# Kernel tuning notes

Measured on AMD Instinct MI355X. Metric: run time of the kernel, lower is better.

## Reference

```python
import jax, jax.numpy as jnp
import numpy as np

B = 1024        # sessions
N = 32          # nodes per session
S = 50          # steps per session
H = 256         # hidden_size
V = 50000       # vocab size of embedding_table
GROUP = 3       # items pooled per step (reshape(-1, 3, H) in source)
SAN_BLOCKS = 3


def setup_inputs() -> dict:
    key = jax.random.key(0)
    ks = jax.random.split(key, 16)
    node_embedding = jax.random.normal(ks[0], (B * N, H), jnp.float32)
    emb_weight = jax.random.normal(ks[1], (V, H), jnp.float32) * 0.02
    batch = jnp.repeat(jnp.arange(B, dtype=jnp.int32), N)           # session id per node
    sequence = jax.random.randint(ks[2], (B * S, GROUP), 0, N + 1)  # local idx; ==N -> zero pad row
    itemset_len = jax.random.randint(ks[3], (B * S,), 1, GROUP + 1).astype(jnp.float32)
    sequence_len = jnp.full((B,), S, dtype=jnp.int32)               # steps per session
    cue = jax.random.randint(ks[4], (B,), 0, V)
    sc = 1.0 / np.sqrt(H)
    in_proj_w = jax.random.normal(ks[5], (3 * H, H), jnp.float32) * sc
    in_proj_b = jnp.zeros((3 * H,), jnp.float32)
    out_proj_w = jax.random.normal(ks[6], (H, H), jnp.float32) * sc
    out_proj_b = jnp.zeros((H,), jnp.float32)
    d1_w = jax.random.normal(ks[7], (H, H), jnp.float32) * sc
    d1_b = jnp.zeros((H,), jnp.float32)
    d2_w = jax.random.normal(ks[8], (H, H), jnp.float32) * sc
    d2_b = jnp.zeros((H,), jnp.float32)
    W3_w = jax.random.normal(ks[9], (H, 2 * H), jnp.float32) * (1.0 / np.sqrt(2 * H))
    W3_b = jnp.zeros((H,), jnp.float32)
    return {
        "node_embedding": node_embedding, "emb_weight": emb_weight,
        "itemset_len": itemset_len, "in_proj_w": in_proj_w, "in_proj_b": in_proj_b,
        "out_proj_w": out_proj_w, "out_proj_b": out_proj_b,
        "d1_w": d1_w, "d1_b": d1_b, "d2_w": d2_w, "d2_b": d2_b,
        "W3_w": W3_w, "W3_b": W3_b,
        "batch": batch, "sequence": sequence, "sequence_len": sequence_len, "cue": cue,
    }


def reference(node_embedding, emb_weight, itemset_len, in_proj_w, in_proj_b,
              out_proj_w, out_proj_b, d1_w, d1_b, d2_w, d2_b, W3_w, W3_b,
              batch, sequence, sequence_len, cue):
    # Eval mode: dropout disabled.
    total_nodes, h = node_embedding.shape
    nsess = sequence_len.shape[0]
    total_steps = sequence.shape[0]

    # Per-session node counts and exclusive offsets (replaces torch.split on ragged batch).
    sections = jnp.bincount(batch, length=nsess)
    offsets = jnp.cumsum(sections) - sections

    # Append one global zero row; local index == sections[sess] maps to it
    # (matches the per-session zero row in v_i_zeros).
    nodes_pad = jnp.concatenate([node_embedding, jnp.zeros((1, h), node_embedding.dtype)], axis=0)
    step_sess = jnp.repeat(jnp.arange(nsess), sequence_len, total_repeat_length=total_steps)
    sec_s = sections[step_sess][:, None]
    off_s = offsets[step_sess][:, None]
    gidx = jnp.where(sequence == sec_s, total_nodes, off_s + sequence)  # [T, 3] global indices

    # session_i: 3-way sum of gathered node embeddings / itemset_len  -> [T, H]
    step_emb = nodes_pad[gidx].sum(axis=1) / itemset_len[:, None]

    # Last step of each session (both v_n and the position s_g is read from).
    last_idx = jnp.cumsum(sequence_len) - 1
    v_n = step_emb[last_idx]  # [B, H]

    # nn.MultiheadAttention receives (L=1, N=steps, E=H): softmax over a single key
    # is identically 1, so MHA == out_proj(v_proj(x)) applied per step independently.
    # Hence the SAN chain on the last step equals the chain applied to v_n alone.
    Wv = in_proj_w[2 * h:]
    bv = in_proj_b[2 * h:]
    x = v_n
    for _ in range(SAN_BLOCKS):
        attn = (x @ Wv.T + bv) @ out_proj_w.T + out_proj_b
        # Residual FFN (dropout off in eval): x + d2(relu(d1(x)))
        x = attn + (jax.nn.relu(attn @ d1_w.T + d1_b) @ d2_w.T + d2_b)
    s_g = x  # [B, H]

    s_h = jnp.concatenate([v_n, s_g], axis=1) @ W3_w.T + W3_b  # [B, H]
    y_hat = jnp.sum(s_h * emb_weight[cue], axis=1)             # [B]
    all_scores = s_h @ emb_weight.T                            # [B, V]
    return y_hat, all_scores
```

## Files before the change

kernel.cpp:

```cpp
#include <hip/hip_runtime.h>
#include <hip/hip_bf16.h>
#include <stdint.h>

typedef __attribute__((ext_vector_type(8))) short short8;
typedef __attribute__((ext_vector_type(4))) short short4v;
typedef __attribute__((ext_vector_type(4))) float f32x4;

#define HD 256

__device__ __forceinline__ ushort f2bf(float f) {
  union { float f; uint32_t u; } x; x.f = f;
  uint32_t r = (x.u + 0x7fffu + ((x.u >> 16) & 1u)) >> 16;
  return (ushort)r;
}

__device__ __forceinline__ int swz(int row, int col) {
  int chunk = (col >> 3) ^ (row & 7);
  return row * 256 + chunk * 8 + (col & 7);
}

__global__ void prep1_kernel(const int* __restrict__ batch, int total_nodes,
                             int* __restrict__ sections,
                             const float* __restrict__ in_proj_w,
                             const float* __restrict__ out_proj_w,
                             const float* __restrict__ d1_w,
                             const float* __restrict__ d2_w,
                             const float* __restrict__ W3_w,
                             ushort* __restrict__ Wv_bf, ushort* __restrict__ Po_bf,
                             ushort* __restrict__ d1_bf, ushort* __restrict__ d2_bf,
                             ushort* __restrict__ W3_bf) {
  int stride = gridDim.x * blockDim.x;
  int t0 = blockIdx.x * blockDim.x + threadIdx.x;
  for (int i = t0; i < total_nodes; i += stride)
    atomicAdd(&sections[batch[i]], 1);
  for (int i = t0; i < HD * HD; i += stride) {
    Wv_bf[i] = f2bf(in_proj_w[2 * HD * HD + i]);
    Po_bf[i] = f2bf(out_proj_w[i]);
    d1_bf[i] = f2bf(d1_w[i]);
    d2_bf[i] = f2bf(d2_w[i]);
  }
  for (int i = t0; i < HD * 2 * HD; i += stride)
    W3_bf[i] = f2bf(W3_w[i]);
}

__global__ void scan_kernel(const int* __restrict__ seq_len, int* __restrict__ sections,
                            int* __restrict__ offsets, int* __restrict__ last_idx,
                            int nsess) {
  __shared__ int s1[1024];
  __shared__ int s2[1024];
  int t = threadIdx.x;
  int v1 = (t < nsess) ? sections[t] : 0;
  int v2 = (t < nsess) ? seq_len[t] : 0;
  s1[t] = v1; s2[t] = v2;
  for (int d = 1; d < 1024; d <<= 1) {
    __syncthreads();
    int a1 = (t >= d) ? s1[t - d] : 0;
    int a2 = (t >= d) ? s2[t - d] : 0;
    __syncthreads();
    s1[t] += a1; s2[t] += a2;
  }
  __syncthreads();
  if (t < nsess) {
    offsets[t] = s1[t] - v1;
    last_idx[t] = s2[t] - 1;
  }
}

template<bool RELU, bool RESID, bool WACC>
__device__ __forceinline__ void gemm_stage16(const ushort* inA, const ushort* __restrict__ Wbf,
                                             const float* __restrict__ bias,
                                             float* accf, ushort* outB) {
  int t = threadIdx.x;
  int lane = t & 63, wid = t >> 6;
  int la = lane & 15, g = lane >> 4;
  int col = wid * 16 + la;
  f32x4 acc = {0.f, 0.f, 0.f, 0.f};
#pragma unroll
  for (int kk = 0; kk < 8; ++kk) {
    short8 a = *(const short8*)&inA[swz(la, kk * 32 + g * 8)];
    short8 b = *(const short8*)&Wbf[col * HD + kk * 32 + g * 8];
    acc = __builtin_amdgcn_mfma_f32_16x16x32_bf16(a, b, acc, 0, 0, 0);
  }
  float bia = bias[col];
#pragma unroll
  for (int r = 0; r < 4; ++r) {
    int ro = g * 4 + r;
    float v = acc[r] + bia;
    if (RELU) v = fmaxf(v, 0.f);
    if (RESID) v += accf[ro * HD + col];
    if (WACC) accf[ro * HD + col] = v;
    outB[swz(ro, col)] = f2bf(v);
  }
}

__device__ __forceinline__ void stage_fence() {
  __syncthreads();
  __builtin_amdgcn_sched_barrier(0);
}

__global__ __launch_bounds__(1024, 1) void sh_kernel(
    const float* __restrict__ node_emb, const float* __restrict__ emb_w,
    const float* __restrict__ itemset_len, const float* __restrict__ in_proj_b,
    const float* __restrict__ out_proj_b, const float* __restrict__ d1_b,
    const float* __restrict__ d2_b, const float* __restrict__ W3_b,
    const int* __restrict__ sequence, const int* __restrict__ cue,
    const int* __restrict__ sections, const int* __restrict__ offsets,
    const int* __restrict__ last_idx,
    const ushort* __restrict__ Wv_bf, const ushort* __restrict__ Po_bf,
    const ushort* __restrict__ d1_bf, const ushort* __restrict__ d2_bf,
    const ushort* __restrict__ W3_bf,
    ushort* __restrict__ sh_bf, float* __restrict__ y_hat, int group) {
  __shared__ float accf[16 * HD];
  __shared__ ushort vn_bf[16 * HD];
  __shared__ ushort bufA[16 * HD];
  __shared__ ushort bufB[16 * HD];
  int t = threadIdx.x;
  int b0 = blockIdx.x * 16;

  {
    int r = t >> 6, cg = t & 63;
    int sess = b0 + r;
    int li = last_idx[sess];
    float inv = 1.0f / itemset_len[li];
    int sec = sections[sess], off = offsets[sess];
    float4 s = {0.f, 0.f, 0.f, 0.f};
    for (int gi = 0; gi < group; ++gi) {
      int sq = sequence[li * group + gi];
      if (sq == sec) continue;
      float4 v = *(const float4*)(node_emb + (size_t)(off + sq) * HD + cg * 4);
      s.x += v.x; s.y += v.y; s.z += v.z; s.w += v.w;
    }
    short4v u;
    u[0] = (short)f2bf(s.x * inv); u[1] = (short)f2bf(s.y * inv);
    u[2] = (short)f2bf(s.z * inv); u[3] = (short)f2bf(s.w * inv);
    *(short4v*)&vn_bf[swz(r, cg * 4)] = u;
  }
  stage_fence();

  const ushort* cur = vn_bf;
#pragma unroll 1
  for (int sb = 0; sb < 3; ++sb) {
    gemm_stage16<false, false, false>(cur, Wv_bf, in_proj_b + 2 * HD, nullptr, bufA);
    stage_fence();
    gemm_stage16<false, false, true>(bufA, Po_bf, out_proj_b, accf, bufB);
    stage_fence();
    gemm_stage16<true, false, false>(bufB, d1_bf, d1_b, nullptr, bufA);
    stage_fence();
    gemm_stage16<false, true, false>(bufA, d2_bf, d2_b, accf, bufB);
    stage_fence();
    cur = bufB;
  }

  {
    int lane = t & 63, wid = t >> 6;
    int la = lane & 15, g = lane >> 4;
    int col = wid * 16 + la;
    f32x4 acc = {0.f, 0.f, 0.f, 0.f};
#pragma unroll
    for (int kk = 0; kk < 16; ++kk) {
      const ushort* src = (kk < 8) ? vn_bf : cur;
      short8 a = *(const short8*)&src[swz(la, (kk & 7) * 32 + g * 8)];
      short8 b = *(const short8*)&W3_bf[col * 2 * HD + kk * 32 + g * 8];
      acc = __builtin_amdgcn_mfma_f32_16x16x32_bf16(a, b, acc, 0, 0, 0);
    }
    float bia = W3_b[col];
#pragma unroll
    for (int r = 0; r < 4; ++r) {
      int ro = g * 4 + r;
      float v = acc[r] + bia;
      accf[ro * HD + col] = v;
      sh_bf[(size_t)(b0 + ro) * HD + col] = f2bf(v);
    }
  }
  stage_fence();

  {
    int r = t >> 6, lane = t & 63;
    const float4 er = *(const float4*)(emb_w + (size_t)cue[b0 + r] * HD + lane * 4);
    const float* ar = &accf[r * HD + lane * 4];
    float p = ar[0] * er.x + ar[1] * er.y + ar[2] * er.z + ar[3] * er.w;
#pragma unroll
    for (int off = 32; off >= 1; off >>= 1) p += __shfl_down(p, off, 64);
    if (lane == 0) y_hat[b0 + r] = p;
  }
}

__global__ __launch_bounds__(256) void score_kernel(
    const ushort* __restrict__ sh_bf, const float* __restrict__ emb_w,
    float* __restrict__ scores, int nrows, int V) {
  __shared__ ushort ebuf[64 * HD];
  int t = threadIdx.x;
  int c0 = blockIdx.x * 64;
#pragma unroll
  for (int i = 0; i < 8; ++i) {
    int c = t + i * 256;
    int row = c >> 5, q = c & 31;
    if (c0 + row < V) {
      const float4* src = (const float4*)(emb_w + (size_t)(c0 + row) * HD + q * 8);
      float4 v0 = src[0], v1 = src[1];
      short8 u;
      u[0] = (short)f2bf(v0.x); u[1] = (short)f2bf(v0.y);
      u[2] = (short)f2bf(v0.z); u[3] = (short)f2bf(v0.w);
      u[4] = (short)f2bf(v1.x); u[5] = (short)f2bf(v1.y);
      u[6] = (short)f2bf(v1.z); u[7] = (short)f2bf(v1.w);
      *(short8*)&ebuf[row * 256 + ((q ^ (row & 7)) * 8)] = u;
    }
  }
  __syncthreads();

  int lane = t & 63, wid = t >> 6;
  int la = lane & 15, g = lane >> 4;
  int nrb = nrows >> 6;
  for (int rb = 0; rb < nrb; ++rb) {
    int r0 = rb * 64 + wid * 16;
    const ushort* arow = sh_bf + (size_t)(r0 + la) * HD;
    short8 a[8];
#pragma unroll
    for (int kk = 0; kk < 8; ++kk) a[kk] = *(const short8*)&arow[kk * 32 + g * 8];
    f32x4 acc[4] = {{0.f,0.f,0.f,0.f},{0.f,0.f,0.f,0.f},{0.f,0.f,0.f,0.f},{0.f,0.f,0.f,0.f}};
#pragma unroll
    for (int kk = 0; kk < 8; ++kk) {
#pragma unroll
      for (int ct = 0; ct < 4; ++ct) {
        int brow = ct * 16 + la;
        short8 b = *(const short8*)&ebuf[brow * 256 + (((kk * 4 + g) ^ (brow & 7)) * 8)];
        acc[ct] = __builtin_amdgcn_mfma_f32_16x16x32_bf16(a[kk], b, acc[ct], 0, 0, 0);
      }
    }
#pragma unroll
    for (int ct = 0; ct < 4; ++ct) {
      int col = c0 + ct * 16 + la;
      if (col < V) {
#pragma unroll
        for (int r = 0; r < 4; ++r) {
          int m = r0 + g * 4 + r;
          scores[(size_t)m * V + col] = acc[ct][r];
        }
      }
    }
  }
}

extern "C" void kernel_launch(void* const* d_in, const int* in_sizes, int n_in,
                              void* d_out, int out_size, void* d_ws, size_t ws_size,
                              hipStream_t stream) {
  const float* node_emb   = (const float*)d_in[0];
  const float* emb_w      = (const float*)d_in[1];
  const float* itemset_len= (const float*)d_in[2];
  const float* in_proj_w  = (const float*)d_in[3];
  const float* in_proj_b  = (const float*)d_in[4];
  const float* out_proj_w = (const float*)d_in[5];
  const float* out_proj_b = (const float*)d_in[6];
  const float* d1_w       = (const float*)d_in[7];
  const float* d1_b       = (const float*)d_in[8];
  const float* d2_w       = (const float*)d_in[9];
  const float* d2_b       = (const float*)d_in[10];
  const float* W3_w       = (const float*)d_in[11];
  const float* W3_b       = (const float*)d_in[12];
  const int*   batch      = (const int*)d_in[13];
  const int*   sequence   = (const int*)d_in[14];
  const int*   seq_len    = (const int*)d_in[15];
  const int*   cue        = (const int*)d_in[16];

  int total_nodes = in_sizes[0] / HD;
  int V           = in_sizes[1] / HD;
  int nsess       = in_sizes[15];
  int total_steps = in_sizes[2];
  int group       = in_sizes[14] / total_steps;

  char* ws = (char*)d_ws;
  int* sections   = (int*)(ws);
  int* offsets    = (int*)(ws + 4096);
  int* last_idx   = (int*)(ws + 8192);
  ushort* sh_bf   = (ushort*)(ws + 16384);
  ushort* Wv_bf   = (ushort*)(ws + 16384 + 524288);
  ushort* Po_bf   = Wv_bf + HD * HD;
  ushort* d1_bf   = Po_bf + HD * HD;
  ushort* d2_bf   = d1_bf + HD * HD;
  ushort* W3_bf   = d2_bf + HD * HD;

  float* y_hat  = (float*)d_out;
  float* scores = (float*)d_out + nsess;

  hipMemsetAsync(sections, 0, (size_t)nsess * sizeof(int), stream);
  prep1_kernel<<<512, 256, 0, stream>>>(batch, total_nodes, sections,
                                        in_proj_w, out_proj_w, d1_w, d2_w, W3_w,
                                        Wv_bf, Po_bf, d1_bf, d2_bf, W3_bf);
  scan_kernel<<<1, 1024, 0, stream>>>(seq_len, sections, offsets, last_idx, nsess);
  sh_kernel<<<nsess / 16, 1024, 0, stream>>>(node_emb, emb_w, itemset_len, in_proj_b,
                                             out_proj_b, d1_b, d2_b, W3_b,
                                             sequence, cue, sections, offsets, last_idx,
                                             Wv_bf, Po_bf, d1_bf, d2_bf, W3_bf,
                                             sh_bf, y_hat, group);
  score_kernel<<<(V + 63) / 64, 256, 0, stream>>>(sh_bf, emb_w, scores, nsess, V);
}
```

Before: 162.8 us.

## Fold V/out projections into one matrix, binary-search sections, vectorize score stores

Precomputes Wc = out_proj·Wv and a combined bias on device, so each SAN block runs three GEMM stages instead of four. Replaces the atomic histogram plus memset for session sizes with a per-session binary search over the sorted batch array. The score kernel now stages MFMA results in shared memory so it can write 16-byte vectorized, row-contiguous stores to the large output. This cuts prep and launch overhead and improves write coalescing, at the cost of extra LDS use and a slightly different bf16 rounding path for the fused matrix.

```diff
diff --git a/kernel.cpp b/kernel.cpp
--- a/kernel.cpp
+++ b/kernel.cpp
@@ -19,49 +19,67 @@
   return row * 256 + chunk * 8 + (col & 7);
 }
 
-__global__ void prep1_kernel(const int* __restrict__ batch, int total_nodes,
-                             int* __restrict__ sections,
-                             const float* __restrict__ in_proj_w,
+__global__ void prep1_kernel(const float* __restrict__ in_proj_w,
+                             const float* __restrict__ in_proj_b,
                              const float* __restrict__ out_proj_w,
+                             const float* __restrict__ out_proj_b,
                              const float* __restrict__ d1_w,
                              const float* __restrict__ d2_w,
                              const float* __restrict__ W3_w,
-                             ushort* __restrict__ Wv_bf, ushort* __restrict__ Po_bf,
-                             ushort* __restrict__ d1_bf, ushort* __restrict__ d2_bf,
-                             ushort* __restrict__ W3_bf) {
-  int stride = gridDim.x * blockDim.x;
-  int t0 = blockIdx.x * blockDim.x + threadIdx.x;
-  for (int i = t0; i < total_nodes; i += stride)
-    atomicAdd(&sections[batch[i]], 1);
-  for (int i = t0; i < HD * HD; i += stride) {
-    Wv_bf[i] = f2bf(in_proj_w[2 * HD * HD + i]);
-    Po_bf[i] = f2bf(out_proj_w[i]);
+                             ushort* __restrict__ Wc_bf, ushort* __restrict__ d1_bf,
+                             ushort* __restrict__ d2_bf, ushort* __restrict__ W3_bf,
+                             float* __restrict__ bc) {
+  int blk = blockIdx.x, t = threadIdx.x;
+  if (blk < 256) {
+    int i = blk * 256 + t;
     d1_bf[i] = f2bf(d1_w[i]);
     d2_bf[i] = f2bf(d2_w[i]);
-  }
-  for (int i = t0; i < HD * 2 * HD; i += stride)
     W3_bf[i] = f2bf(W3_w[i]);
-}
-
-__global__ void scan_kernel(const int* __restrict__ seq_len, int* __restrict__ sections,
-                            int* __restrict__ offsets, int* __restrict__ last_idx,
-                            int nsess) {
-  __shared__ int s1[1024];
+    W3_bf[i + 65536] = f2bf(W3_w[i + 65536]);
+  } else {
+    int i = blk - 256;
+    const float* Po = out_proj_w + i * HD;
+    const float* Wv = in_proj_w + 2 * HD * HD;
+    float acc = 0.f;
+    for (int m = 0; m < HD; ++m) acc += Po[m] * Wv[m * HD + t];
+    Wc_bf[i * HD + t] = f2bf(acc);
+    if (t == 0) {
+      const float* bv = in_proj_b + 2 * HD;
+      float b = out_proj_b[i];
+      for (int m = 0; m < HD; ++m) b += Po[m] * bv[m];
+      bc[i] = b;
+    }
+  }
+}
+
+__global__ void scan_kernel(const int* __restrict__ batch, int total_nodes,
+                            const int* __restrict__ seq_len,
+                            int* __restrict__ sections, int* __restrict__ offsets,
+                            int* __restrict__ last_idx, int nsess) {
+  __shared__ int lbs[1025];
   __shared__ int s2[1024];
   int t = threadIdx.x;
-  int v1 = (t < nsess) ? sections[t] : 0;
+  if (t < nsess) {
+    int lo = 0, hi = total_nodes;
+    while (lo < hi) {
+      int mid = (lo + hi) >> 1;
+      if (batch[mid] < t) lo = mid + 1; else hi = mid;
+    }
+    lbs[t] = lo;
+  }
+  if (t == 0) lbs[nsess] = total_nodes;
   int v2 = (t < nsess) ? seq_len[t] : 0;
-  s1[t] = v1; s2[t] = v2;
+  s2[t] = v2;
   for (int d = 1; d < 1024; d <<= 1) {
     __syncthreads();
-    int a1 = (t >= d) ? s1[t - d] : 0;
     int a2 = (t >= d) ? s2[t - d] : 0;
     __syncthreads();
-    s1[t] += a1; s2[t] += a2;
+    s2[t] += a2;
   }
   __syncthreads();
   if (t < nsess) {
-    offsets[t] = s1[t] - v1;
+    offsets[t] = lbs[t];
+    sections[t] = lbs[t + 1] - lbs[t];
     last_idx[t] = s2[t] - 1;
   }
 }
@@ -100,15 +118,14 @@
 
 __global__ __launch_bounds__(1024, 1) void sh_kernel(
     const float* __restrict__ node_emb, const float* __restrict__ emb_w,
-    const float* __restrict__ itemset_len, const float* __restrict__ in_proj_b,
-    const float* __restrict__ out_proj_b, const float* __restrict__ d1_b,
-    const float* __restrict__ d2_b, const float* __restrict__ W3_b,
+    const float* __restrict__ itemset_len,
+    const float* __restrict__ d1_b, const float* __restrict__ d2_b,
+    const float* __restrict__ W3_b, const float* __restrict__ bc,
     const int* __restrict__ sequence, const int* __restrict__ cue,
     const int* __restrict__ sections, const int* __restrict__ offsets,
     const int* __restrict__ last_idx,
-    const ushort* __restrict__ Wv_bf, const ushort* __restrict__ Po_bf,
-    const ushort* __restrict__ d1_bf, const ushort* __restrict__ d2_bf,
-    const ushort* __restrict__ W3_bf,
+    const ushort* __restrict__ Wc_bf, const ushort* __restrict__ d1_bf,
+    const ushort* __restrict__ d2_bf, const ushort* __restrict__ W3_bf,
     ushort* __restrict__ sh_bf, float* __restrict__ y_hat, int group) {
   __shared__ float accf[16 * HD];
   __shared__ ushort vn_bf[16 * HD];
@@ -137,18 +154,19 @@
   }
   stage_fence();
 
-  const ushort* cur = vn_bf;
+  const ushort* x = vn_bf;
+  ushort* P = bufA;
+  ushort* Q = bufB;
 #pragma unroll 1
   for (int sb = 0; sb < 3; ++sb) {
-    gemm_stage16<false, false, false>(cur, Wv_bf, in_proj_b + 2 * HD, nullptr, bufA);
+    gemm_stage16<false, false, true>(x, Wc_bf, bc, accf, P);
     stage_fence();
-    gemm_stage16<false, false, true>(bufA, Po_bf, out_proj_b, accf, bufB);
+    gemm_stage16<true, false, false>(P, d1_bf, d1_b, nullptr, Q);
     stage_fence();
-    gemm_stage16<true, false, false>(bufB, d1_bf, d1_b, nullptr, bufA);
+    gemm_stage16<false, true, false>(Q, d2_bf, d2_b, accf, P);
     stage_fence();
-    gemm_stage16<false, true, false>(bufA, d2_bf, d2_b, accf, bufB);
-    stage_fence();
-    cur = bufB;
+    x = P;
+    ushort* tmp = P; P = Q; Q = tmp;
   }
 
   {
@@ -158,7 +176,7 @@
     f32x4 acc = {0.f, 0.f, 0.f, 0.f};
 #pragma unroll
     for (int kk = 0; kk < 16; ++kk) {
-      const ushort* src = (kk < 8) ? vn_bf : cur;
+      const ushort* src = (kk < 8) ? vn_bf : x;
       short8 a = *(const short8*)&src[swz(la, (kk & 7) * 32 + g * 8)];
       short8 b = *(const short8*)&W3_bf[col * 2 * HD + kk * 32 + g * 8];
       acc = __builtin_amdgcn_mfma_f32_16x16x32_bf16(a, b, acc, 0, 0, 0);
@@ -189,6 +207,7 @@
     const ushort* __restrict__ sh_bf, const float* __restrict__ emb_w,
     float* __restrict__ scores, int nrows, int V) {
   __shared__ ushort ebuf[64 * HD];
+  __shared__ float obuf[4][16][68];
   int t = threadIdx.x;
   int c0 = blockIdx.x * 64;
 #pragma unroll
@@ -210,6 +229,9 @@
 
   int lane = t & 63, wid = t >> 6;
   int la = lane & 15, g = lane >> 4;
+  int colf = lane & 15;
+  int rquad = lane >> 4;
+  bool cok = (c0 + colf * 4) < V;
   int nrb = nrows >> 6;
   for (int rb = 0; rb < nrb; ++rb) {
     int r0 = rb * 64 + wid * 16;
@@ -228,15 +250,16 @@
       }
     }
 #pragma unroll
-    for (int ct = 0; ct < 4; ++ct) {
-      int col = c0 + ct * 16 + la;
-      if (col < V) {
-#pragma unroll
-        for (int r = 0; r < 4; ++r) {
-          int m = r0 + g * 4 + r;
-          scores[(size_t)m * V + col] = acc[ct][r];
-        }
-      }
+    for (int ct = 0; ct < 4; ++ct)
+#pragma unroll
+      for (int r = 0; r < 4; ++r)
+        obuf[wid][g * 4 + r][ct * 16 + la] = acc[ct][r];
+#pragma unroll
+    for (int i = 0; i < 4; ++i) {
+      int row = i * 4 + rquad;
+      f32x4 v = *(const f32x4*)&obuf[wid][row][colf * 4];
+      if (cok)
+        *(f32x4*)&scores[(size_t)(r0 + row) * V + c0 + colf * 4] = v;
     }
   }
 }
@@ -272,25 +295,25 @@
   int* sections   = (int*)(ws);
   int* offsets    = (int*)(ws + 4096);
   int* last_idx   = (int*)(ws + 8192);
+  float* bc       = (float*)(ws + 12288);
   ushort* sh_bf   = (ushort*)(ws + 16384);
-  ushort* Wv_bf   = (ushort*)(ws + 16384 + 524288);
-  ushort* Po_bf   = Wv_bf + HD * HD;
-  ushort* d1_bf   = Po_bf + HD * HD;
+  ushort* Wc_bf   = (ushort*)(ws + 16384 + 524288);
+  ushort* d1_bf   = Wc_bf + HD * HD;
   ushort* d2_bf   = d1_bf + HD * HD;
   ushort* W3_bf   = d2_bf + HD * HD;
 
   float* y_hat  = (float*)d_out;
   float* scores = (float*)d_out + nsess;
 
-  hipMemsetAsync(sections, 0, (size_t)nsess * sizeof(int), stream);
-  prep1_kernel<<<512, 256, 0, stream>>>(batch, total_nodes, sections,
-                                        in_proj_w, out_proj_w, d1_w, d2_w, W3_w,
-                                        Wv_bf, Po_bf, d1_bf, d2_bf, W3_bf);
-  scan_kernel<<<1, 1024, 0, stream>>>(seq_len, sections, offsets, last_idx, nsess);
-  sh_kernel<<<nsess / 16, 1024, 0, stream>>>(node_emb, emb_w, itemset_len, in_proj_b,
-                                             out_proj_b, d1_b, d2_b, W3_b,
+  prep1_kernel<<<512, 256, 0, stream>>>(in_proj_w, in_proj_b, out_proj_w, out_proj_b,
+                                        d1_w, d2_w, W3_w,
+                                        Wc_bf, d1_bf, d2_bf, W3_bf, bc);
+  scan_kernel<<<1, 1024, 0, stream>>>(batch, total_nodes, seq_len,
+                                      sections, offsets, last_idx, nsess);
+  sh_kernel<<<nsess / 16, 1024, 0, stream>>>(node_emb, emb_w, itemset_len,
+                                             d1_b, d2_b, W3_b, bc,
                                              sequence, cue, sections, offsets, last_idx,
-                                             Wv_bf, Po_bf, d1_bf, d2_bf, W3_bf,
+                                             Wc_bf, d1_bf, d2_bf, W3_bf,
                                              sh_bf, y_hat, group);
   score_kernel<<<(V + 63) / 64, 256, 0, stream>>>(sh_bf, emb_w, scores, nsess, V);
 }
```

New measurement: 141.2 us. 1.15x faster.
